# Performance work log

Hardware: AMD Instinct MI355X
Metric: run time of the kernel (lower is better)

## Reference

```python
import jax, jax.numpy as jnp
import numpy as np

B, D = 16384, 1024


def setup_inputs() -> dict:
    key = jax.random.key(0)
    ks = jax.random.split(key, 6)
    s = 1.0 / np.sqrt(D)  # glorot-ish scale for theta vectors
    return {
        "enc_user": jax.random.normal(ks[0], (B, D), dtype=jnp.float32),
        "enc_item": jax.random.normal(ks[1], (B, D), dtype=jnp.float32),
        "theta_vv": jax.random.normal(ks[2], (1, D, 1), dtype=jnp.float32) * s,
        "theta_ev": jax.random.normal(ks[3], (1, D, 1), dtype=jnp.float32) * s,
        "theta_ve": jax.random.normal(ks[4], (1, D, 1), dtype=jnp.float32) * s,
        "theta_ee": jax.random.normal(ks[5], (1, D, 1), dtype=jnp.float32) * s,
        "beta_v": jnp.zeros((1, D, 1), dtype=jnp.float32),
        "beta_e": jnp.zeros((1, D, 1), dtype=jnp.float32),
    }


def reference(enc_user, enc_item, theta_vv, theta_ev, theta_ve, theta_ee, beta_v, beta_e):
    # Cross matrix C = v e^T (B, D, D); C @ theta and C^T @ theta contract to
    # scaled copies of v and e:  C @ t = v * (e . t),  C^T @ t = e * (v . t).
    t_vv, t_ev = theta_vv[0, :, 0], theta_ev[0, :, 0]
    t_ve, t_ee = theta_ve[0, :, 0], theta_ee[0, :, 0]
    b_v, b_e = beta_v[0, :, 0], beta_e[0, :, 0]

    e_vv = (enc_item @ t_vv)[:, None]  # (B, 1)
    v_ev = (enc_user @ t_ev)[:, None]
    e_ve = (enc_item @ t_ve)[:, None]
    v_ee = (enc_user @ t_ee)[:, None]

    v_out = enc_user * e_vv + enc_item * v_ev + b_v  # (B, D)
    e_out = enc_user * e_ve + enc_item * v_ee + b_e  # (B, D)
    return v_out, e_out
```

## Files before the change

### kernel.cpp

```cpp
#include <hip/hip_runtime.h>

#define BB 16384
#define DD 1024

typedef float f32x4 __attribute__((ext_vector_type(4)));

__global__ __launch_bounds__(256) void cross_compress_kernel(
    const float* __restrict__ enc_user,
    const float* __restrict__ enc_item,
    const float* __restrict__ t_vv,
    const float* __restrict__ t_ev,
    const float* __restrict__ t_ve,
    const float* __restrict__ t_ee,
    const float* __restrict__ b_v,
    const float* __restrict__ b_e,
    float* __restrict__ out)
{
    const int row  = blockIdx.x;
    const int tid  = threadIdx.x;
    const int c    = tid << 2;
    const long base = (long)row * DD;

    const f32x4 u  = *reinterpret_cast<const f32x4*>(enc_user + base + c);
    const f32x4 it = *reinterpret_cast<const f32x4*>(enc_item + base + c);
    const f32x4 vv = *reinterpret_cast<const f32x4*>(t_vv + c);
    const f32x4 ev = *reinterpret_cast<const f32x4*>(t_ev + c);
    const f32x4 ve = *reinterpret_cast<const f32x4*>(t_ve + c);
    const f32x4 ee = *reinterpret_cast<const f32x4*>(t_ee + c);

    float s0 = it.x*vv.x + it.y*vv.y + it.z*vv.z + it.w*vv.w;
    float s1 =  u.x*ev.x +  u.y*ev.y +  u.z*ev.z +  u.w*ev.w;
    float s2 = it.x*ve.x + it.y*ve.y + it.z*ve.z + it.w*ve.w;
    float s3 =  u.x*ee.x +  u.y*ee.y +  u.z*ee.z +  u.w*ee.w;

    #pragma unroll
    for (int off = 32; off > 0; off >>= 1) {
        s0 += __shfl_xor(s0, off);
        s1 += __shfl_xor(s1, off);
        s2 += __shfl_xor(s2, off);
        s3 += __shfl_xor(s3, off);
    }

    __shared__ float red[4][4];
    const int wave = tid >> 6;
    if ((tid & 63) == 0) {
        red[wave][0] = s0; red[wave][1] = s1;
        red[wave][2] = s2; red[wave][3] = s3;
    }
    __syncthreads();

    const float e_vv = red[0][0] + red[1][0] + red[2][0] + red[3][0];
    const float v_ev = red[0][1] + red[1][1] + red[2][1] + red[3][1];
    const float e_ve = red[0][2] + red[1][2] + red[2][2] + red[3][2];
    const float v_ee = red[0][3] + red[1][3] + red[2][3] + red[3][3];

    const f32x4 bv = *reinterpret_cast<const f32x4*>(b_v + c);
    const f32x4 be = *reinterpret_cast<const f32x4*>(b_e + c);

    f32x4 vo, eo;
    vo.x = u.x*e_vv + it.x*v_ev + bv.x;
    vo.y = u.y*e_vv + it.y*v_ev + bv.y;
    vo.z = u.z*e_vv + it.z*v_ev + bv.z;
    vo.w = u.w*e_vv + it.w*v_ev + bv.w;

    eo.x = u.x*e_ve + it.x*v_ee + be.x;
    eo.y = u.y*e_ve + it.y*v_ee + be.y;
    eo.z = u.z*e_ve + it.z*v_ee + be.z;
    eo.w = u.w*e_ve + it.w*v_ee + be.w;

    __builtin_nontemporal_store(vo, reinterpret_cast<f32x4*>(out + base + c));
    __builtin_nontemporal_store(eo, reinterpret_cast<f32x4*>(out + (long)BB * DD + base + c));
}

extern "C" void kernel_launch(void* const* d_in, const int* in_sizes, int n_in,
                              void* d_out, int out_size, void* d_ws, size_t ws_size,
                              hipStream_t stream) {
    const float* enc_user = (const float*)d_in[0];
    const float* enc_item = (const float*)d_in[1];
    const float* t_vv     = (const float*)d_in[2];
    const float* t_ev     = (const float*)d_in[3];
    const float* t_ve     = (const float*)d_in[4];
    const float* t_ee     = (const float*)d_in[5];
    const float* b_v      = (const float*)d_in[6];
    const float* b_e      = (const float*)d_in[7];
    float* out = (float*)d_out;

    dim3 grid(BB);
    dim3 block(256);
    cross_compress_kernel<<<grid, block, 0, stream>>>(
        enc_user, enc_item, t_vv, t_ev, t_ve, t_ee, b_v, b_e, out);
}
```

Measured before the change: 43.42 us.

## Map one wavefront per row with persistent grid-stride loop

Each wavefront now processes a whole row with four float4 chunks per lane and reduces via shuffles only, eliminating the shared-memory reduction and block barrier. A fixed grid of 1024 blocks loops over rows, loading theta and bias vectors into registers once per wave. This trades barrier and redundant constant loads for higher register pressure and fewer concurrent waves, which may reduce memory-level parallelism.

```diff
diff --git a/kernel.cpp b/kernel.cpp
--- a/kernel.cpp
+++ b/kernel.cpp
@@ -1,9 +1,11 @@
 #include <hip/hip_runtime.h>
+
+typedef float f32x4 __attribute__((ext_vector_type(4)));
 
 #define BB 16384
 #define DD 1024
-
-typedef float f32x4 __attribute__((ext_vector_type(4)));
+#define NBLK 1024
+#define NWAVES (NBLK * 4)
 
 __global__ __launch_bounds__(256) void cross_compress_kernel(
     const float* __restrict__ enc_user,
@@ -16,60 +18,67 @@
     const float* __restrict__ b_e,
     float* __restrict__ out)
 {
-    const int row  = blockIdx.x;
     const int tid  = threadIdx.x;
-    const int c    = tid << 2;
-    const long base = (long)row * DD;
+    const int lane = tid & 63;
+    const int gw   = blockIdx.x * 4 + (tid >> 6);
+    const int c0   = lane << 2;
 
-    const f32x4 u  = *reinterpret_cast<const f32x4*>(enc_user + base + c);
-    const f32x4 it = *reinterpret_cast<const f32x4*>(enc_item + base + c);
-    const f32x4 vv = *reinterpret_cast<const f32x4*>(t_vv + c);
-    const f32x4 ev = *reinterpret_cast<const f32x4*>(t_ev + c);
-    const f32x4 ve = *reinterpret_cast<const f32x4*>(t_ve + c);
-    const f32x4 ee = *reinterpret_cast<const f32x4*>(t_ee + c);
-
-    float s0 = it.x*vv.x + it.y*vv.y + it.z*vv.z + it.w*vv.w;
-    float s1 =  u.x*ev.x +  u.y*ev.y +  u.z*ev.z +  u.w*ev.w;
-    float s2 = it.x*ve.x + it.y*ve.y + it.z*ve.z + it.w*ve.w;
-    float s3 =  u.x*ee.x +  u.y*ee.y +  u.z*ee.z +  u.w*ee.w;
-
+    f32x4 vv[4], ev[4], ve[4], ee[4], bv[4], be[4];
     #pragma unroll
-    for (int off = 32; off > 0; off >>= 1) {
-        s0 += __shfl_xor(s0, off);
-        s1 += __shfl_xor(s1, off);
-        s2 += __shfl_xor(s2, off);
-        s3 += __shfl_xor(s3, off);
+    for (int k = 0; k < 4; ++k) {
+        const int c = c0 + 256 * k;
+        vv[k] = *reinterpret_cast<const f32x4*>(t_vv + c);
+        ev[k] = *reinterpret_cast<const f32x4*>(t_ev + c);
+        ve[k] = *reinterpret_cast<const f32x4*>(t_ve + c);
+        ee[k] = *reinterpret_cast<const f32x4*>(t_ee + c);
+        bv[k] = *reinterpret_cast<const f32x4*>(b_v + c);
+        be[k] = *reinterpret_cast<const f32x4*>(b_e + c);
     }
 
-    __shared__ float red[4][4];
-    const int wave = tid >> 6;
-    if ((tid & 63) == 0) {
-        red[wave][0] = s0; red[wave][1] = s1;
-        red[wave][2] = s2; red[wave][3] = s3;
+    for (int r = gw; r < BB; r += NWAVES) {
+        const long base = (long)r * DD;
+
+        f32x4 u[4], it[4];
+        #pragma unroll
+        for (int k = 0; k < 4; ++k) {
+            u[k]  = *reinterpret_cast<const f32x4*>(enc_user + base + c0 + 256 * k);
+            it[k] = *reinterpret_cast<const f32x4*>(enc_item + base + c0 + 256 * k);
+        }
+
+        float s0 = 0.f, s1 = 0.f, s2 = 0.f, s3 = 0.f;
+        #pragma unroll
+        for (int k = 0; k < 4; ++k) {
+            s0 += it[k].x*vv[k].x + it[k].y*vv[k].y + it[k].z*vv[k].z + it[k].w*vv[k].w;
+            s1 +=  u[k].x*ev[k].x +  u[k].y*ev[k].y +  u[k].z*ev[k].z +  u[k].w*ev[k].w;
+            s2 += it[k].x*ve[k].x + it[k].y*ve[k].y + it[k].z*ve[k].z + it[k].w*ve[k].w;
+            s3 +=  u[k].x*ee[k].x +  u[k].y*ee[k].y +  u[k].z*ee[k].z +  u[k].w*ee[k].w;
+        }
+
+        #pragma unroll
+        for (int off = 32; off > 0; off >>= 1) {
+            s0 += __shfl_xor(s0, off);
+            s1 += __shfl_xor(s1, off);
+            s2 += __shfl_xor(s2, off);
+            s3 += __shfl_xor(s3, off);
+        }
+
+        #pragma unroll
+        for (int k = 0; k < 4; ++k) {
+            f32x4 vo, eo;
+            vo.x = u[k].x*s0 + it[k].x*s1 + bv[k].x;
+            vo.y = u[k].y*s0 + it[k].y*s1 + bv[k].y;
+            vo.z = u[k].z*s0 + it[k].z*s1 + bv[k].z;
+            vo.w = u[k].w*s0 + it[k].w*s1 + bv[k].w;
+            eo.x = u[k].x*s2 + it[k].x*s3 + be[k].x;
+            eo.y = u[k].y*s2 + it[k].y*s3 + be[k].y;
+            eo.z = u[k].z*s2 + it[k].z*s3 + be[k].z;
+            eo.w = u[k].w*s2 + it[k].w*s3 + be[k].w;
+            __builtin_nontemporal_store(vo,
+                reinterpret_cast<f32x4*>(out + base + c0 + 256 * k));
+            __builtin_nontemporal_store(eo,
+                reinterpret_cast<f32x4*>(out + (long)BB * DD + base + c0 + 256 * k));
+        }
     }
-    __syncthreads();
-
-    const float e_vv = red[0][0] + red[1][0] + red[2][0] + red[3][0];
-    const float v_ev = red[0][1] + red[1][1] + red[2][1] + red[3][1];
-    const float e_ve = red[0][2] + red[1][2] + red[2][2] + red[3][2];
-    const float v_ee = red[0][3] + red[1][3] + red[2][3] + red[3][3];
-
-    const f32x4 bv = *reinterpret_cast<const f32x4*>(b_v + c);
-    const f32x4 be = *reinterpret_cast<const f32x4*>(b_e + c);
-
-    f32x4 vo, eo;
-    vo.x = u.x*e_vv + it.x*v_ev + bv.x;
-    vo.y = u.y*e_vv + it.y*v_ev + bv.y;
-    vo.z = u.z*e_vv + it.z*v_ev + bv.z;
-    vo.w = u.w*e_vv + it.w*v_ev + bv.w;
-
-    eo.x = u.x*e_ve + it.x*v_ee + be.x;
-    eo.y = u.y*e_ve + it.y*v_ee + be.y;
-    eo.z = u.z*e_ve + it.z*v_ee + be.z;
-    eo.w = u.w*e_ve + it.w*v_ee + be.w;
-
-    __builtin_nontemporal_store(vo, reinterpret_cast<f32x4*>(out + base + c));
-    __builtin_nontemporal_store(eo, reinterpret_cast<f32x4*>(out + (long)BB * DD + base + c));
 }
 
 extern "C" void kernel_launch(void* const* d_in, const int* in_sizes, int n_in,
@@ -85,8 +94,6 @@
     const float* b_e      = (const float*)d_in[7];
     float* out = (float*)d_out;
 
-    dim3 grid(BB);
-    dim3 block(256);
-    cross_compress_kernel<<<grid, block, 0, stream>>>(
+    cross_compress_kernel<<<dim3(NBLK), dim3(256), 0, stream>>>(
         enc_user, enc_item, t_vv, t_ev, t_ve, t_ee, b_v, b_e, out);
 }
```

Result: slower. 47.10 us (+8.5%).
